# Kernel tuning notes

Measured on AMD Instinct MI355X. Metric: run time of the kernel, lower is better.

## Reference

```python
import jax, jax.numpy as jnp
import numpy as np

BAND_WIDTHS = [16]*20 + [32]*12 + [64]*4 + [65]
B, C, F, T, E = 4, 2, 1025, 2048, 128
MAX_BW = 65
D = C * MAX_BW * 2  # padded feature dim (in_channels * max_bandwidth * reim)
EPS = 1e-5


def _band_meta():
    widths = np.asarray(BAND_WIDTHS, np.int32)
    starts = np.concatenate([[0], np.cumsum(widths)[:-1]]).astype(np.int32)
    nb = len(widths)
    bw_mask = (np.arange(MAX_BW)[None, :] < widths[:, None])  # [nb, MAX_BW]
    # feature order per band is (channel, bw, reim), matching torch view_as_real+reshape
    feat_mask = np.broadcast_to(bw_mask[:, None, :, None], (nb, C, MAX_BW, 2)).reshape(nb, D)
    return starts, widths, feat_mask.astype(np.float32)


def setup_inputs() -> dict:
    key = jax.random.key(0)
    ks = jax.random.split(key, 6)
    starts, widths, feat_mask = _band_meta()
    nb = len(widths)
    fm = jnp.asarray(feat_mask)
    x = jax.random.normal(ks[0], (B, C, F, T, 2), jnp.float32)
    ln_gamma = (1.0 + 0.1 * jax.random.normal(ks[1], (nb, D), jnp.float32)) * fm
    ln_beta = 0.1 * jax.random.normal(ks[2], (nb, D), jnp.float32) * fm
    v = 0.05 * jax.random.normal(ks[3], (nb, E, D), jnp.float32) * fm[:, None, :]
    g = 1.0 + 0.1 * jax.random.normal(ks[4], (nb, E), jnp.float32)
    bias = 0.05 * jax.random.normal(ks[5], (nb, E), jnp.float32)
    return {
        "x": x, "ln_gamma": ln_gamma, "ln_beta": ln_beta, "v": v, "g": g,
        "bias": bias, "band_start": jnp.asarray(starts), "band_width": jnp.asarray(widths),
    }


def reference(x, ln_gamma, ln_beta, v, g, bias, band_start, band_width):
    nb = band_start.shape[0]
    # padded gather of each band's frequency slice
    idx = jnp.clip(band_start[:, None] + jnp.arange(MAX_BW)[None, :], 0, F - 1)  # [nb, MAX_BW]
    xb = jnp.take(x, idx, axis=2)               # [B, C, nb, MAX_BW, T, 2]
    xb = jnp.transpose(xb, (0, 2, 4, 1, 3, 5))  # [B, nb, T, C, MAX_BW, 2]
    xb = xb.reshape(B, nb, T, D)
    bw_mask = (jnp.arange(MAX_BW)[None, :] < band_width[:, None])
    fm = jnp.broadcast_to(bw_mask[:, None, :, None], (nb, C, MAX_BW, 2)).reshape(nb, D).astype(x.dtype)
    m = fm[None, :, None, :]                    # [1, nb, 1, D]
    n = (band_width * C * 2).astype(x.dtype)[None, :, None]  # true norm_in per band
    # masked LayerNorm over the valid (ragged) features of each band
    mean = jnp.sum(xb * m, axis=-1) / n         # [B, nb, T]
    diff = (xb - mean[..., None]) * m
    var = jnp.sum(diff * diff, axis=-1) / n
    xhat = diff * jax.lax.rsqrt(var + EPS)[..., None]
    y = (xhat * ln_gamma[None, :, None, :] + ln_beta[None, :, None, :]) * m
    # weight-normalized Linear: W = g * V / ||V||_row (padded cols of V are zero)
    vnorm = jnp.sqrt(jnp.sum(v * v, axis=-1, keepdims=True))  # [nb, E, 1]
    W = g[..., None] * v / vnorm
    z = jnp.einsum("bntd,ned->bnte", y, W) + bias[:, None, :]  # [B, nb, T, E]
    return z
```

## Files before the change

### kernel.cpp

```cpp
#include <hip/hip_runtime.h>
#include <math.h>

#define NB 37
#define BB 4
#define CC 2
#define FF 1025
#define TT 2048
#define EE 128
#define DD 260
#define EPSF 1e-5f
#define CHS 9

typedef short s16x8 __attribute__((ext_vector_type(8)));
typedef float f32x4 __attribute__((ext_vector_type(4)));
typedef const unsigned int __attribute__((address_space(1))) gu32;
typedef unsigned int __attribute__((address_space(3))) lu32;

__device__ __forceinline__ unsigned short f2bf(float f) {
    unsigned u = __builtin_bit_cast(unsigned, f);
    unsigned r = (u + 0x7FFFu + ((u >> 16) & 1u)) >> 16;
    return (unsigned short)r;
}

__global__ __launch_bounds__(256) void prep_kernel(
    const float* __restrict__ gamma, const float* __restrict__ beta,
    const float* __restrict__ v, const float* __restrict__ g,
    const float* __restrict__ bias, const int* __restrict__ bwidth,
    unsigned short* __restrict__ ATg, float* __restrict__ s1o, float* __restrict__ s2o)
{
    int bid = blockIdx.x;
    int n   = bid >> 4;
    int eg  = bid & 15;
    int tid = threadIdx.x;
    int el  = tid >> 5;
    int kk  = tid & 31;
    int e   = eg * 8 + el;

    int bw    = bwidth[n];
    int Deff  = 4 * bw;
    int twobw = 2 * bw;
    int nCh   = (Deff + 31) >> 5;

    const float* vp = v + (size_t)(n * EE + e) * DD;

    float sq = 0.f;
    for (int d = kk; d < DD; d += 32) { float val = vp[d]; sq = fmaf(val, val, sq); }
    #pragma unroll
    for (int m = 16; m >= 1; m >>= 1) sq += __shfl_xor(sq, m);

    float rv = g[n * EE + e] * rsqrtf(sq);

    float s1 = 0.f, s2 = 0.f;
    unsigned short* Abase = ATg + (size_t)n * CHS * (EE * 32) + e * 32 + kk;
    for (int ch = 0; ch < nCh; ++ch) {
        int k = ch * 32 + kk;
        float a = 0.f;
        if (k < Deff) {
            int d = (k >= twobw) ? (130 + k - twobw) : k;
            float W = rv * vp[d];
            a = gamma[n * DD + d] * W;
            s1 += a;
            s2 = fmaf(beta[n * DD + d], W, s2);
        }
        Abase[(size_t)ch * (EE * 32)] = f2bf(a);
    }
    #pragma unroll
    for (int m = 16; m >= 1; m >>= 1) { s1 += __shfl_xor(s1, m); s2 += __shfl_xor(s2, m); }
    if (kk == 0) {
        s1o[n * EE + e] = s1;
        s2o[n * EE + e] = s2 + bias[n * EE + e];
    }
}

__global__ __launch_bounds__(256, 3) void fused_kernel(
    const float* __restrict__ x, const int* __restrict__ bstart,
    const int* __restrict__ bwidth,
    const unsigned short* __restrict__ ATg, const float* __restrict__ s1a,
    const float* __restrict__ s2a, float* __restrict__ out)
{
    int bid  = blockIdx.x;
    int n    = bid % NB;
    int rest = bid / NB;
    int tt   = rest & 15;
    int b    = rest >> 4;
    int t0   = tt * 128;
    int f0   = bstart[n];
    int bw   = bwidth[n];
    int nPairs = 2 * bw;
    int Deff   = 4 * bw;
    int nChF   = Deff >> 5;
    int remP   = nPairs - nChF * 16;
    int nChT   = nChF + (remP ? 1 : 0);

    int tid   = threadIdx.x;
    int lane  = tid & 63;
    int l15   = lane & 15;
    int ksub  = lane >> 4;
    int wv    = tid >> 6;
    int tband = (wv >> 1) * 64;
    int ewave = (wv & 1) * 64;

    __shared__ __align__(16) float Xs[2][16 * 256];

    const char* xbase = (const char*)x;

    auto STAGE = [&](int ch, int bufIdx) {
        #pragma unroll
        for (int j = 0; j < 4; ++j) {
            int pl = wv * 4 + j;
            int p  = ch * 16 + pl;
            p = (p < nPairs) ? p : (nPairs - 1);
            int c   = (p >= bw) ? 1 : 0;
            int row = (b * CC + c) * FF + f0 + (p - c * bw);
            const char* gsrc = xbase + (size_t)row * 16384 + (size_t)t0 * 8
                             + (size_t)lane * 16;
            __builtin_amdgcn_global_load_lds(
                (gu32*)gsrc, (lu32*)&Xs[bufIdx][pl * 256], 16, 0, 0);
        }
    };

    const s16x8* Ab = reinterpret_cast<const s16x8*>(
        ATg + (size_t)n * CHS * (EE * 32)) + ((ewave + l15) * 4 + ksub);

    f32x4 acc[4][4];
    #pragma unroll
    for (int mi = 0; mi < 4; ++mi)
        #pragma unroll
        for (int ni = 0; ni < 4; ++ni)
            acc[mi][ni] = (f32x4){0.f, 0.f, 0.f, 0.f};
    float sA[4] = {0.f, 0.f, 0.f, 0.f};
    float qA[4] = {0.f, 0.f, 0.f, 0.f};

    STAGE(0, 0);
    __syncthreads();

    for (int ch = 0; ch < nChT; ++ch) {
        s16x8 a0 = Ab[ch * 512];
        s16x8 a1 = Ab[ch * 512 + 64];
        s16x8 a2 = Ab[ch * 512 + 128];
        s16x8 a3 = Ab[ch * 512 + 192];

        if (ch + 1 < nChT) STAGE(ch + 1, (ch + 1) & 1);

        const float2* Xp = reinterpret_cast<const float2*>(&Xs[ch & 1][0]);
        bool tail = (ch == nChF);

        #pragma unroll
        for (int mi = 0; mi < 4; ++mi) {
            float2 vv[4];
            #pragma unroll
            for (int j = 0; j < 4; ++j)
                vv[j] = Xp[(4 * ksub + j) * 128 + tband + mi * 16 + l15];
            if (tail) {
                #pragma unroll
                for (int j = 0; j < 4; ++j)
                    if (4 * ksub + j >= remP) vv[j] = make_float2(0.f, 0.f);
            }
            float s = 0.f, q = 0.f;
            s16x8 af;
            #pragma unroll
            for (int j = 0; j < 4; ++j) {
                s += vv[j].x + vv[j].y;
                q = fmaf(vv[j].x, vv[j].x, q);
                q = fmaf(vv[j].y, vv[j].y, q);
                af[2 * j]     = (short)f2bf(vv[j].x);
                af[2 * j + 1] = (short)f2bf(vv[j].y);
            }
            sA[mi] += s;
            qA[mi] += q;
            acc[mi][0] = __builtin_amdgcn_mfma_f32_16x16x32_bf16(af, a0, acc[mi][0], 0, 0, 0);
            acc[mi][1] = __builtin_amdgcn_mfma_f32_16x16x32_bf16(af, a1, acc[mi][1], 0, 0, 0);
            acc[mi][2] = __builtin_amdgcn_mfma_f32_16x16x32_bf16(af, a2, acc[mi][2], 0, 0, 0);
            acc[mi][3] = __builtin_amdgcn_mfma_f32_16x16x32_bf16(af, a3, acc[mi][3], 0, 0, 0);
        }
        __syncthreads();
    }

    float inv = 1.f / (float)Deff;
    float mrow[4][4], rrow[4][4];
    #pragma unroll
    for (int mi = 0; mi < 4; ++mi) {
        float s = sA[mi], q = qA[mi];
        s += __shfl_xor(s, 16); s += __shfl_xor(s, 32);
        q += __shfl_xor(q, 16); q += __shfl_xor(q, 32);
        float mean = s * inv;
        float var  = fmaf(q, inv, -mean * mean);
        float rs   = rsqrtf(var + EPSF);
        #pragma unroll
        for (int j = 0; j < 4; ++j) {
            int src = (ksub << 2) + j;
            mrow[mi][j] = __shfl(mean, src);
            rrow[mi][j] = __shfl(rs, src);
        }
    }

    float s1r[4], s2r[4];
    #pragma unroll
    for (int ni = 0; ni < 4; ++ni) {
        int e = ewave + ni * 16 + l15;
        s1r[ni] = s1a[n * EE + e];
        s2r[ni] = s2a[n * EE + e];
    }
    size_t outRow = ((size_t)(b * NB + n)) * TT;
    #pragma unroll
    for (int mi = 0; mi < 4; ++mi) {
        #pragma unroll
        for (int j = 0; j < 4; ++j) {
            int t = t0 + tband + mi * 16 + (ksub << 2) + j;
            float m = mrow[mi][j], r = rrow[mi][j];
            float* op = out + (outRow + t) * EE + ewave + l15;
            #pragma unroll
            for (int ni = 0; ni < 4; ++ni)
                op[ni * 16] = fmaf(r, acc[mi][ni][j] - m * s1r[ni], s2r[ni]);
        }
    }
}

extern "C" void kernel_launch(void* const* d_in, const int* in_sizes, int n_in,
                              void* d_out, int out_size, void* d_ws, size_t ws_size,
                              hipStream_t stream)
{
    const float* x      = (const float*)d_in[0];
    const float* gamma  = (const float*)d_in[1];
    const float* beta   = (const float*)d_in[2];
    const float* v      = (const float*)d_in[3];
    const float* g      = (const float*)d_in[4];
    const float* bias   = (const float*)d_in[5];
    const int*   bstart = (const int*)d_in[6];
    const int*   bwidth = (const int*)d_in[7];
    float* out = (float*)d_out;

    unsigned short* ATg = (unsigned short*)d_ws;
    float* s1  = (float*)(ATg + (size_t)NB * CHS * EE * 32);
    float* s2p = s1 + NB * EE;

    prep_kernel<<<NB * 16, 256, 0, stream>>>(gamma, beta, v, g, bias, bwidth, ATg, s1, s2p);
    fused_kernel<<<BB * NB * 16, 256, 0, stream>>>(x, bstart, bwidth, ATg, s1, s2p, out);
}
```

Before: 82.29 us.

## Template per band width and process four time slabs per block

The fused kernel is templated on band width so chunk counts and tail handling are compile-time constants. Each block now loops over four 128-step time slabs, launching a quarter as many blocks. Weight fragments are kept in registers for narrow bands, and staging of the next slab overlaps with compute across slab boundaries. The MFMA operands are swapped so accumulators map to contiguous E, allowing float4 output stores, and blocks are ordered widest band first. Fewer blocks may reduce parallelism and load balance across CUs.

```diff
diff --git a/kernel.cpp b/kernel.cpp
--- a/kernel.cpp
+++ b/kernel.cpp
@@ -3,7 +3,6 @@
 
 #define NB 37
 #define BB 4
-#define CC 2
 #define FF 1025
 #define TT 2048
 #define EE 128
@@ -72,148 +71,168 @@
     }
 }
 
-__global__ __launch_bounds__(256, 3) void fused_kernel(
+template <int BW>
+__device__ __forceinline__ void run_band(
+    const float* __restrict__ x, const unsigned short* __restrict__ ATg,
+    const float* __restrict__ s1a, const float* __restrict__ s2a,
+    float* __restrict__ out, float* __restrict__ Xs,
+    int b, int n, int tslab0, int f0, int tid)
+{
+    constexpr int  NCH   = (4 * BW + 31) / 32;
+    constexpr bool TAIL  = (BW == 65);
+    constexpr bool ARES  = (BW <= 32);
+    constexpr int  NPAIR = 2 * BW;
+    constexpr int  REMP  = NPAIR - (NCH - 1) * 16;
+
+    const int lane  = tid & 63;
+    const int l15   = lane & 15;
+    const int ksub  = lane >> 4;
+    const int wv    = tid >> 6;
+    const int tband = (wv >> 1) * 64;
+    const int ewave = (wv & 1) * 64;
+
+    const s16x8* Ab = reinterpret_cast<const s16x8*>(
+        ATg + (size_t)n * CHS * (EE * 32)) + ((ewave + l15) * 4 + ksub);
+
+    s16x8 afr[ARES ? NCH : 1][4];
+    if (ARES) {
+        #pragma unroll
+        for (int ch = 0; ch < NCH; ++ch)
+            #pragma unroll
+            for (int ni = 0; ni < 4; ++ni)
+                afr[ch][ni] = Ab[ch * 512 + ni * 64];
+    }
+
+    const char* xb = (const char*)x + (size_t)(b * 2) * FF * 16384
+                   + (size_t)tslab0 * 8 + (size_t)lane * 16;
+
+    auto STAGE = [&](int ts, int ch, int bufOff) {
+        #pragma unroll
+        for (int j = 0; j < 4; ++j) {
+            int p = ch * 16 + wv * 4 + j;
+            if (TAIL && p > NPAIR - 1) p = NPAIR - 1;
+            int c = (p >= BW) ? 1 : 0;
+            int row = c * FF + f0 + p - c * BW;
+            const char* gsrc = xb + (size_t)row * 16384 + (size_t)ts * 1024;
+            __builtin_amdgcn_global_load_lds((gu32*)gsrc,
+                (lu32*)(Xs + bufOff + (wv * 4 + j) * 256), 16, 0, 0);
+        }
+    };
+
+    STAGE(0, 0, 0);
+    __syncthreads();
+
+    f32x4 acc[4][4];
+    #pragma unroll
+    for (int mi = 0; mi < 4; ++mi)
+        #pragma unroll
+        for (int ni = 0; ni < 4; ++ni) acc[mi][ni] = (f32x4){0.f, 0.f, 0.f, 0.f};
+    float sA[4] = {0.f, 0.f, 0.f, 0.f}, qA[4] = {0.f, 0.f, 0.f, 0.f};
+
+    int bufOff = 0;
+    for (int ts = 0; ts < 4; ++ts) {
+        #pragma unroll
+        for (int ch = 0; ch < NCH; ++ch) {
+            s16x8 aw0, aw1, aw2, aw3;
+            if (ARES) {
+                aw0 = afr[ch][0]; aw1 = afr[ch][1]; aw2 = afr[ch][2]; aw3 = afr[ch][3];
+            } else {
+                aw0 = Ab[ch * 512];       aw1 = Ab[ch * 512 + 64];
+                aw2 = Ab[ch * 512 + 128]; aw3 = Ab[ch * 512 + 192];
+            }
+            int nbuf = bufOff ^ 4096;
+            if (ch + 1 < NCH)      STAGE(ts, ch + 1, nbuf);
+            else if (ts + 1 < 4)   STAGE(ts + 1, 0, nbuf);
+
+            const float2* Xp = reinterpret_cast<const float2*>(Xs + bufOff);
+            #pragma unroll
+            for (int mi = 0; mi < 4; ++mi) {
+                float2 vv[4];
+                #pragma unroll
+                for (int j = 0; j < 4; ++j)
+                    vv[j] = Xp[(4 * ksub + j) * 128 + tband + mi * 16 + l15];
+                if (TAIL && ch == NCH - 1) {
+                    #pragma unroll
+                    for (int j = 0; j < 4; ++j)
+                        if (4 * ksub + j >= REMP) vv[j] = make_float2(0.f, 0.f);
+                }
+                float s = 0.f, q = 0.f;
+                s16x8 af;
+                #pragma unroll
+                for (int j = 0; j < 4; ++j) {
+                    s += vv[j].x + vv[j].y;
+                    q = fmaf(vv[j].x, vv[j].x, q);
+                    q = fmaf(vv[j].y, vv[j].y, q);
+                    af[2 * j]     = (short)f2bf(vv[j].x);
+                    af[2 * j + 1] = (short)f2bf(vv[j].y);
+                }
+                sA[mi] += s;
+                qA[mi] += q;
+                acc[mi][0] = __builtin_amdgcn_mfma_f32_16x16x32_bf16(aw0, af, acc[mi][0], 0, 0, 0);
+                acc[mi][1] = __builtin_amdgcn_mfma_f32_16x16x32_bf16(aw1, af, acc[mi][1], 0, 0, 0);
+                acc[mi][2] = __builtin_amdgcn_mfma_f32_16x16x32_bf16(aw2, af, acc[mi][2], 0, 0, 0);
+                acc[mi][3] = __builtin_amdgcn_mfma_f32_16x16x32_bf16(aw3, af, acc[mi][3], 0, 0, 0);
+            }
+            __syncthreads();
+            bufOff ^= 4096;
+        }
+
+        constexpr float inv = 1.f / (float)(4 * BW);
+        size_t outT = (size_t)(b * NB + n) * TT + tslab0 + ts * 128;
+        #pragma unroll
+        for (int mi = 0; mi < 4; ++mi) {
+            float s = sA[mi], q = qA[mi];
+            s += __shfl_xor(s, 16); s += __shfl_xor(s, 32);
+            q += __shfl_xor(q, 16); q += __shfl_xor(q, 32);
+            float mean = s * inv;
+            float rs   = rsqrtf(fmaf(q, inv, -(mean * mean)) + EPSF);
+            float* op = out + (outT + tband + mi * 16 + l15) * EE + ewave + ksub * 4;
+            #pragma unroll
+            for (int ni = 0; ni < 4; ++ni) {
+                float4 s1q = *reinterpret_cast<const float4*>(
+                    &s1a[n * EE + ewave + ni * 16 + ksub * 4]);
+                float4 s2q = *reinterpret_cast<const float4*>(
+                    &s2a[n * EE + ewave + ni * 16 + ksub * 4]);
+                f32x4 a = acc[mi][ni];
+                float4 z;
+                z.x = fmaf(rs, a[0] - mean * s1q.x, s2q.x);
+                z.y = fmaf(rs, a[1] - mean * s1q.y, s2q.y);
+                z.z = fmaf(rs, a[2] - mean * s1q.z, s2q.z);
+                z.w = fmaf(rs, a[3] - mean * s1q.w, s2q.w);
+                *reinterpret_cast<float4*>(op + ni * 16) = z;
+                acc[mi][ni] = (f32x4){0.f, 0.f, 0.f, 0.f};
+            }
+            sA[mi] = 0.f; qA[mi] = 0.f;
+        }
+    }
+}
+
+__global__ __launch_bounds__(256) void fused_kernel(
     const float* __restrict__ x, const int* __restrict__ bstart,
     const int* __restrict__ bwidth,
     const unsigned short* __restrict__ ATg, const float* __restrict__ s1a,
     const float* __restrict__ s2a, float* __restrict__ out)
 {
-    int bid  = blockIdx.x;
-    int n    = bid % NB;
-    int rest = bid / NB;
-    int tt   = rest & 15;
-    int b    = rest >> 4;
-    int t0   = tt * 128;
-    int f0   = bstart[n];
-    int bw   = bwidth[n];
-    int nPairs = 2 * bw;
-    int Deff   = 4 * bw;
-    int nChF   = Deff >> 5;
-    int remP   = nPairs - nChF * 16;
-    int nChT   = nChF + (remP ? 1 : 0);
-
-    int tid   = threadIdx.x;
-    int lane  = tid & 63;
-    int l15   = lane & 15;
-    int ksub  = lane >> 4;
-    int wv    = tid >> 6;
-    int tband = (wv >> 1) * 64;
-    int ewave = (wv & 1) * 64;
-
-    __shared__ __align__(16) float Xs[2][16 * 256];
-
-    const char* xbase = (const char*)x;
-
-    auto STAGE = [&](int ch, int bufIdx) {
-        #pragma unroll
-        for (int j = 0; j < 4; ++j) {
-            int pl = wv * 4 + j;
-            int p  = ch * 16 + pl;
-            p = (p < nPairs) ? p : (nPairs - 1);
-            int c   = (p >= bw) ? 1 : 0;
-            int row = (b * CC + c) * FF + f0 + (p - c * bw);
-            const char* gsrc = xbase + (size_t)row * 16384 + (size_t)t0 * 8
-                             + (size_t)lane * 16;
-            __builtin_amdgcn_global_load_lds(
-                (gu32*)gsrc, (lu32*)&Xs[bufIdx][pl * 256], 16, 0, 0);
-        }
-    };
-
-    const s16x8* Ab = reinterpret_cast<const s16x8*>(
-        ATg + (size_t)n * CHS * (EE * 32)) + ((ewave + l15) * 4 + ksub);
-
-    f32x4 acc[4][4];
-    #pragma unroll
-    for (int mi = 0; mi < 4; ++mi)
-        #pragma unroll
-        for (int ni = 0; ni < 4; ++ni)
-            acc[mi][ni] = (f32x4){0.f, 0.f, 0.f, 0.f};
-    float sA[4] = {0.f, 0.f, 0.f, 0.f};
-    float qA[4] = {0.f, 0.f, 0.f, 0.f};
-
-    STAGE(0, 0);
-    __syncthreads();
-
-    for (int ch = 0; ch < nChT; ++ch) {
-        s16x8 a0 = Ab[ch * 512];
-        s16x8 a1 = Ab[ch * 512 + 64];
-        s16x8 a2 = Ab[ch * 512 + 128];
-        s16x8 a3 = Ab[ch * 512 + 192];
-
-        if (ch + 1 < nChT) STAGE(ch + 1, (ch + 1) & 1);
-
-        const float2* Xp = reinterpret_cast<const float2*>(&Xs[ch & 1][0]);
-        bool tail = (ch == nChF);
-
-        #pragma unroll
-        for (int mi = 0; mi < 4; ++mi) {
-            float2 vv[4];
-            #pragma unroll
-            for (int j = 0; j < 4; ++j)
-                vv[j] = Xp[(4 * ksub + j) * 128 + tband + mi * 16 + l15];
-            if (tail) {
-                #pragma unroll
-                for (int j = 0; j < 4; ++j)
-                    if (4 * ksub + j >= remP) vv[j] = make_float2(0.f, 0.f);
-            }
-            float s = 0.f, q = 0.f;
-            s16x8 af;
-            #pragma unroll
-            for (int j = 0; j < 4; ++j) {
-                s += vv[j].x + vv[j].y;
-                q = fmaf(vv[j].x, vv[j].x, q);
-                q = fmaf(vv[j].y, vv[j].y, q);
-                af[2 * j]     = (short)f2bf(vv[j].x);
-                af[2 * j + 1] = (short)f2bf(vv[j].y);
-            }
-            sA[mi] += s;
-            qA[mi] += q;
-            acc[mi][0] = __builtin_amdgcn_mfma_f32_16x16x32_bf16(af, a0, acc[mi][0], 0, 0, 0);
-            acc[mi][1] = __builtin_amdgcn_mfma_f32_16x16x32_bf16(af, a1, acc[mi][1], 0, 0, 0);
-            acc[mi][2] = __builtin_amdgcn_mfma_f32_16x16x32_bf16(af, a2, acc[mi][2], 0, 0, 0);
-            acc[mi][3] = __builtin_amdgcn_mfma_f32_16x16x32_bf16(af, a3, acc[mi][3], 0, 0, 0);
-        }
-        __syncthreads();
-    }
-
-    float inv = 1.f / (float)Deff;
-    float mrow[4][4], rrow[4][4];
-    #pragma unroll
-    for (int mi = 0; mi < 4; ++mi) {
-        float s = sA[mi], q = qA[mi];
-        s += __shfl_xor(s, 16); s += __shfl_xor(s, 32);
-        q += __shfl_xor(q, 16); q += __shfl_xor(q, 32);
-        float mean = s * inv;
-        float var  = fmaf(q, inv, -mean * mean);
-        float rs   = rsqrtf(var + EPSF);
-        #pragma unroll
-        for (int j = 0; j < 4; ++j) {
-            int src = (ksub << 2) + j;
-            mrow[mi][j] = __shfl(mean, src);
-            rrow[mi][j] = __shfl(rs, src);
-        }
-    }
-
-    float s1r[4], s2r[4];
-    #pragma unroll
-    for (int ni = 0; ni < 4; ++ni) {
-        int e = ewave + ni * 16 + l15;
-        s1r[ni] = s1a[n * EE + e];
-        s2r[ni] = s2a[n * EE + e];
-    }
-    size_t outRow = ((size_t)(b * NB + n)) * TT;
-    #pragma unroll
-    for (int mi = 0; mi < 4; ++mi) {
-        #pragma unroll
-        for (int j = 0; j < 4; ++j) {
-            int t = t0 + tband + mi * 16 + (ksub << 2) + j;
-            float m = mrow[mi][j], r = rrow[mi][j];
-            float* op = out + (outRow + t) * EE + ewave + l15;
-            #pragma unroll
-            for (int ni = 0; ni < 4; ++ni)
-                op[ni * 16] = fmaf(r, acc[mi][ni][j] - m * s1r[ni], s2r[ni]);
-        }
-    }
+    __shared__ __align__(16) float Xs[2 * 4096];
+
+    int bid = blockIdx.x;
+    int r   = bid % NB;
+    int n   = NB - 1 - r;
+    int q2  = bid / NB;
+    int tslab0 = (q2 & 3) * 512;
+    int b   = q2 >> 2;
+    int f0  = bstart[n];
+    int bw  = bwidth[n];
+    int tid = threadIdx.x;
+
+    if (bw == 16)
+        run_band<16>(x, ATg, s1a, s2a, out, Xs, b, n, tslab0, f0, tid);
+    else if (bw == 32)
+        run_band<32>(x, ATg, s1a, s2a, out, Xs, b, n, tslab0, f0, tid);
+    else if (bw == 64)
+        run_band<64>(x, ATg, s1a, s2a, out, Xs, b, n, tslab0, f0, tid);
+    else
+        run_band<65>(x, ATg, s1a, s2a, out, Xs, b, n, tslab0, f0, tid);
 }
 
 extern "C" void kernel_launch(void* const* d_in, const int* in_sizes, int n_in,
@@ -235,5 +254,5 @@
     float* s2p = s1 + NB * EE;
 
     prep_kernel<<<NB * 16, 256, 0, stream>>>(gamma, beta, v, g, bias, bwidth, ATg, s1, s2p);
-    fused_kernel<<<BB * NB * 16, 256, 0, stream>>>(x, bstart, bwidth, ATg, s1, s2p, out);
-}
+    fused_kernel<<<BB * NB * 4, 256, 0, stream>>>(x, bstart, bwidth, ATg, s1, s2p, out);
+}
```

Result: slower. 126.8 us (+54.0%).
